# Optimization experiments

Hardware: AMD Instinct MI355X
Metric: run time of the kernel (lower is better)

The kernel has to match this reference:

```python
import jax, jax.numpy as jnp
import numpy as np

EMBED_DIM = 1024
NUM_HEADS = 16
HEAD_DIM = EMBED_DIM // NUM_HEADS
B, S = 2, 2048


def setup_inputs() -> dict:
    key = jax.random.key(0)
    ks = jax.random.split(key, 9)
    d = EMBED_DIM
    scale = 1.0 / np.sqrt(d)
    inp = {
        "x": jax.random.normal(ks[0], (B, S, d), dtype=jnp.float32),
        "mask": jnp.ones((B, S), dtype=jnp.int32),
        "Wq": jax.random.normal(ks[1], (d, d), dtype=jnp.float32) * scale,
        "bq": jnp.zeros((d,), dtype=jnp.float32),
        "Wk": jax.random.normal(ks[2], (d, d), dtype=jnp.float32) * scale,
        "bk": jnp.zeros((d,), dtype=jnp.float32),
        "Wv": jax.random.normal(ks[3], (d, d), dtype=jnp.float32) * scale,
        "bv": jnp.zeros((d,), dtype=jnp.float32),
        "Wo": jax.random.normal(ks[4], (d, d), dtype=jnp.float32) * scale,
        "bo": jnp.zeros((d,), dtype=jnp.float32),
    }
    return inp


def reference(x, mask, Wq, bq, Wk, bk, Wv, bv, Wo, bo):
    b, s, _ = x.shape
    # projections; torch Linear computes x @ W.T + b
    q = (x @ Wq.T + bq).reshape(b, s, NUM_HEADS, HEAD_DIM).transpose(0, 2, 1, 3)
    k = (x @ Wk.T + bk).reshape(b, s, NUM_HEADS, HEAD_DIM).transpose(0, 2, 1, 3)
    v = (x @ Wv.T + bv).reshape(b, s, NUM_HEADS, HEAD_DIM).transpose(0, 2, 1, 3)
    scores = jnp.einsum("bhqd,bhkd->bhqk", q, k) / np.sqrt(HEAD_DIM)  # (B,H,S,S)
    m = (mask == 0)[:, None, None, :]  # broadcast over heads and query pos
    scores = jnp.where(m, jnp.float32(-1e9), scores)
    attn = jax.nn.softmax(scores, axis=-1)
    out = jnp.einsum("bhqk,bhkd->bhqd", attn, v)
    out = out.transpose(0, 2, 1, 3).reshape(b, s, EMBED_DIM)
    return out @ Wo.T + bo
```

## Files before the change

### kernel.cpp

```cpp
#include <hip/hip_runtime.h>

#define EMBED 1024
#define NHEAD 16
#define HDIM  64
#define BB    2
#define SS    2048

typedef __bf16 bf16x8 __attribute__((ext_vector_type(8)));
typedef float  f32x4  __attribute__((ext_vector_type(4)));
typedef _Float16 f16x8 __attribute__((ext_vector_type(8)));
typedef __fp16 hf16x2 __attribute__((ext_vector_type(2)));

#if defined(__has_builtin)
#if __has_builtin(__builtin_amdgcn_exp2f)
#define EXP2(x) __builtin_amdgcn_exp2f(x)
#else
#define EXP2(x) exp2f(x)
#endif
#else
#define EXP2(x) exp2f(x)
#endif

__device__ __forceinline__ unsigned short f2bf(float f) {
  union { float f; unsigned u; } v; v.f = f;
  unsigned r = v.u + 0x7fffu + ((v.u >> 16) & 1u);
  return (unsigned short)(r >> 16);
}

__device__ __forceinline__ float bf2f(unsigned short u) {
  union { unsigned u; float f; } v; v.u = ((unsigned)u) << 16;
  return v.f;
}

__device__ __forceinline__ unsigned short f2h(float f) {
  union { _Float16 h; unsigned short u; } t;
  t.h = (_Float16)f;
  return t.u;
}

__device__ __forceinline__ void g2l16(const unsigned short* g, unsigned short* l) {
  __builtin_amdgcn_global_load_lds(
      (const __attribute__((address_space(1))) unsigned int*)g,
      (__attribute__((address_space(3))) unsigned int*)l, 16, 0, 0);
}

__global__ __launch_bounds__(256)
void cvt5_kernel(const float* __restrict__ x,  const float* __restrict__ Wq,
                 const float* __restrict__ Wk, const float* __restrict__ Wv,
                 const float* __restrict__ Wo, const int* __restrict__ mask,
                 unsigned short* __restrict__ xb,  unsigned short* __restrict__ Wqb,
                 unsigned short* __restrict__ Wkb, unsigned short* __restrict__ Wvb,
                 unsigned short* __restrict__ Wob, float* __restrict__ mbias) {
  const int i = blockIdx.x * 256 + threadIdx.x;
  if (i < (1 << 21)) {
    const float* src;
    unsigned short* dst;
    int j;
    if (i < (1 << 20)) {
      src = x; dst = xb; j = i;
    } else {
      const int t = i - (1 << 20);
      const int r = t >> 18;
      j = t & ((1 << 18) - 1);
      src = (r == 0) ? Wq : (r == 1) ? Wk : (r == 2) ? Wv : Wo;
      dst = (r == 0) ? Wqb : (r == 1) ? Wkb : (r == 2) ? Wvb : Wob;
    }
    const float4 f = ((const float4*)src)[j];
    ushort4 u;
    u.x = f2bf(f.x); u.y = f2bf(f.y); u.z = f2bf(f.z); u.w = f2bf(f.w);
    ((ushort4*)dst)[j] = u;
  } else {
    const int j = i - (1 << 21);
    const int4 m = ((const int4*)mask)[j];
    float4 o;
    o.x = m.x ? 0.f : -1e30f; o.y = m.y ? 0.f : -1e30f;
    o.z = m.z ? 0.f : -1e30f; o.w = m.w ? 0.f : -1e30f;
    ((float4*)mbias)[j] = o;
  }
}

template <typename EpiFn>
__device__ __forceinline__
void gemm_core(const unsigned short* __restrict__ A,
               const unsigned short* __restrict__ Bm,
               int m0, int n0, EpiFn epi) {
  __shared__ unsigned short sA[128 * 64];
  __shared__ unsigned short sB[128 * 64];
  const int tid = threadIdx.x;
  const int l  = tid & 63;
  const int w  = tid >> 6;
  const int lm = l & 15;
  const int qd = l >> 4;
  const int wm = w & 1;
  const int wn = w >> 1;

  f32x4 acc[4][4];
#pragma unroll
  for (int i = 0; i < 4; ++i)
#pragma unroll
    for (int j = 0; j < 4; ++j) acc[i][j] = (f32x4){0.f, 0.f, 0.f, 0.f};

  for (int k0 = 0; k0 < EMBED; k0 += 64) {
#pragma unroll
    for (int i = 0; i < 4; ++i) {
      const int t = i * 256 + tid;
      const int r = t >> 3;
      const int c = (t & 7) ^ (r & 7);
      g2l16(A + (m0 + r) * EMBED + k0 + c * 8, &sA[(i * 256 + (w << 6)) * 8]);
      g2l16(Bm + (n0 + r) * EMBED + k0 + c * 8, &sB[(i * 256 + (w << 6)) * 8]);
    }
    __syncthreads();
#pragma unroll
    for (int kk = 0; kk < 2; ++kk) {
      bf16x8 af[4], bfr[4];
#pragma unroll
      for (int mi = 0; mi < 4; ++mi) {
        const int R = wm * 64 + mi * 16 + lm;
        const int ch = R * 8 + (((kk << 2) + qd) ^ (R & 7));
        af[mi] = *(const bf16x8*)&sA[ch * 8];
      }
#pragma unroll
      for (int ni = 0; ni < 4; ++ni) {
        const int R = wn * 64 + ni * 16 + lm;
        const int ch = R * 8 + (((kk << 2) + qd) ^ (R & 7));
        bfr[ni] = *(const bf16x8*)&sB[ch * 8];
      }
#pragma unroll
      for (int mi = 0; mi < 4; ++mi)
#pragma unroll
        for (int ni = 0; ni < 4; ++ni)
          acc[mi][ni] = __builtin_amdgcn_mfma_f32_16x16x32_bf16(
              af[mi], bfr[ni], acc[mi][ni], 0, 0, 0);
    }
    __syncthreads();
  }

#pragma unroll
  for (int mi = 0; mi < 4; ++mi)
#pragma unroll
    for (int ni = 0; ni < 4; ++ni) {
      const int mb = m0 + wm * 64 + mi * 16 + qd * 4;
      const int n  = n0 + wn * 64 + ni * 16 + lm;
      epi(acc[mi][ni], mb, n);
    }
}

__device__ __forceinline__ void decode_tile(int flat, int& a0, int& b0) {
  const int sub = flat & 15;
  const int g = flat >> 4;
  a0 = ((g >> 2) * 2 + (sub >> 3));
  b0 = ((g & 3) * 8 + (sub & 7));
}

__global__ __launch_bounds__(256)
void gemm_qkv(const unsigned short* __restrict__ xb,
              const unsigned short* __restrict__ Wqb,
              const unsigned short* __restrict__ Wkb,
              const unsigned short* __restrict__ Wvb,
              const float* __restrict__ bq, const float* __restrict__ bk,
              const float* __restrict__ bv,
              unsigned short* __restrict__ Qb, unsigned short* __restrict__ Kb,
              unsigned short* __restrict__ VTb) {
  const int z = blockIdx.y;
  int a0, b0;
  decode_tile(blockIdx.x, a0, b0);
  if (z < 2) {
    const unsigned short* A = z ? Wkb : Wqb;
    const float* bias = z ? bk : bq;
    unsigned short* O = z ? Kb : Qb;
    const float scale = z ? 1.0f : 0.125f * 1.4426950408889634f;
    gemm_core(A, xb, a0 * 128, b0 * 128, [&](const f32x4& v, int mb, int n) {
      const float4 bvv = *(const float4*)&bias[mb];
      const int h = mb >> 6, d0 = mb & 63;
      const int b = n >> 11, s = n & 2047;
      int sw = s;
      if (z == 1)
        sw = (s & ~31) | (((s >> 2) & 1) << 4) | (((s >> 3) & 3) << 2) | (s & 3);
      ushort4 u;
      u.x = f2bf((v.x + bvv.x) * scale); u.y = f2bf((v.y + bvv.y) * scale);
      u.z = f2bf((v.z + bvv.z) * scale); u.w = f2bf((v.w + bvv.w) * scale);
      *(ushort4*)&O[(((b * NHEAD + h) * SS) + sw) * HDIM + d0] = u;
    });
  } else {
    gemm_core(xb, Wvb, b0 * 128, a0 * 128, [&](const f32x4& v, int mb, int n) {
      const float bvv = bv[n];
      const int b = mb >> 11, s = mb & 2047;
      const int h = n >> 6, d = n & 63;
      ushort4 u;
      u.x = f2h(v.x + bvv); u.y = f2h(v.y + bvv);
      u.z = f2h(v.z + bvv); u.w = f2h(v.w + bvv);
      *(ushort4*)&VTb[(((b * NHEAD + h) * HDIM) + d) * SS + s] = u;
    });
  }
}

__global__ __launch_bounds__(256)
void gemm_out(const unsigned short* __restrict__ Wob,
              const unsigned short* __restrict__ Ob,
              const float* __restrict__ bo, float* __restrict__ out) {
  int a0, b0;
  decode_tile(blockIdx.x, a0, b0);
  gemm_core(Wob, Ob, a0 * 128, b0 * 128, [&](const f32x4& v, int mb, int n) {
    const float4 bvv = *(const float4*)&bo[mb];
    float4 o;
    o.x = v.x + bvv.x; o.y = v.y + bvv.y; o.z = v.z + bvv.z; o.w = v.w + bvv.w;
    *(float4*)&out[n * EMBED + mb] = o;
  });
}

__global__ __launch_bounds__(256, 6)
void attn_kernel(const unsigned short* __restrict__ Q,
                 const unsigned short* __restrict__ K,
                 const unsigned short* __restrict__ VT,
                 const float* __restrict__ mbias,
                 unsigned short* __restrict__ Opart,
                 float* __restrict__ Lpart) {
  __shared__ unsigned short sK[64 * 64];
  __shared__ unsigned short sV[64 * 64];
  __shared__ float sMB[SS / 2];
  const int tid = threadIdx.x;
  const int l = tid & 63, w = tid >> 6;
  const int lm = l & 15, qd = l >> 4;
  const int b = blockIdx.z & 1, sp = blockIdx.z >> 1, h = blockIdx.y;
  const int q0 = blockIdx.x * 64 + w * 16;
  const unsigned short* Qh = Q + ((b * NHEAD + h) * SS) * HDIM;
  const unsigned short* Kh = K + ((b * NHEAD + h) * SS) * HDIM;
  const unsigned short* Vh = VT + ((b * NHEAD + h) * HDIM) * SS;
  const float* mb = mbias + b * SS + sp * (SS / 2);
  unsigned short* Op = Opart + sp * (BB * SS * EMBED);
  float* Lp = Lpart + sp * (BB * NHEAD * SS);
  const int kb0 = sp * (SS / 2);

  bf16x8 qf[2];
  qf[0] = *(const bf16x8*)&Qh[(q0 + lm) * HDIM + qd * 8];
  qf[1] = *(const bf16x8*)&Qh[(q0 + lm) * HDIM + 32 + qd * 8];

  auto stageKV = [&](int kb) {
#pragma unroll
    for (int i = 0; i < 2; ++i) {
      const int t = i * 256 + tid;
      const int r = t >> 3;
      const int c = (t & 7) ^ (r & 7);
      g2l16(Kh + (kb + r) * HDIM + c * 8, &sK[(i * 256 + (w << 6)) * 8]);
      g2l16(Vh + r * SS + kb + c * 8, &sV[(i * 256 + (w << 6)) * 8]);
    }
  };

  g2l16((const unsigned short*)(mb + tid * 4), (unsigned short*)&sMB[w * 256]);

  f32x4 Od[4];
#pragma unroll
  for (int i = 0; i < 4; ++i) Od[i] = (f32x4){0.f, 0.f, 0.f, 0.f};
  float lsum = 0.f;

  const int NT = (SS / 2) / 64;
  for (int t = 0; t < NT; ++t) {
    stageKV(kb0 + t * 64);
    __syncthreads();

#pragma unroll
    for (int p = 0; p < 2; ++p) {
      union PK { hf16x2 h2[4]; f16x8 v; } pk;
#pragma unroll
      for (int jj = 0; jj < 2; ++jj) {
        const int j = p * 2 + jj;
        const int R = j * 16 + lm;
        const bf16x8 k0 = *(const bf16x8*)&sK[(R * 8 + (qd ^ (lm & 7))) * 8];
        const bf16x8 k1 = *(const bf16x8*)&sK[(R * 8 + ((4 + qd) ^ (lm & 7))) * 8];
        const float4 bj = *(const float4*)&sMB[t * 64 + p * 32 + qd * 8 + jj * 4];
        f32x4 t0 = (f32x4){bj.x, bj.y, bj.z, bj.w};
        __builtin_amdgcn_s_setprio(1);
        t0 = __builtin_amdgcn_mfma_f32_16x16x32_bf16(k0, qf[0], t0, 0, 0, 0);
        t0 = __builtin_amdgcn_mfma_f32_16x16x32_bf16(k1, qf[1], t0, 0, 0, 0);
        __builtin_amdgcn_s_setprio(0);
        const float p0 = EXP2(t0[0]);
        const float p1 = EXP2(t0[1]);
        const float p2 = EXP2(t0[2]);
        const float p3 = EXP2(t0[3]);
        lsum += (p0 + p1) + (p2 + p3);
        pk.h2[jj * 2] = __builtin_amdgcn_cvt_pkrtz(p0, p1);
        pk.h2[jj * 2 + 1] = __builtin_amdgcn_cvt_pkrtz(p2, p3);
      }
      const f16x8 pf8 = pk.v;
      __builtin_amdgcn_s_setprio(1);
#pragma unroll
      for (int dt = 0; dt < 4; ++dt) {
        const f16x8 vf =
            *(const f16x8*)&sV[(dt * 16 + lm) * 64 + ((p * 4 + qd) ^ (lm & 7)) * 8];
        Od[dt] = __builtin_amdgcn_mfma_f32_16x16x32_f16(vf, pf8, Od[dt], 0, 0, 0);
      }
      __builtin_amdgcn_s_setprio(0);
    }
    __syncthreads();
  }

  float ls = lsum;
  ls += __shfl_xor(ls, 16);
  ls += __shfl_xor(ls, 32);
  if (qd == 0) Lp[(b * NHEAD + h) * SS + q0 + lm] = ls;
#pragma unroll
  for (int dt = 0; dt < 4; ++dt) {
    ushort4 u;
    u.x = f2bf(Od[dt][0]); u.y = f2bf(Od[dt][1]);
    u.z = f2bf(Od[dt][2]); u.w = f2bf(Od[dt][3]);
    *(ushort4*)&Op[(b * SS + q0 + lm) * EMBED + h * HDIM + dt * 16 + qd * 4] = u;
  }
}

__global__ __launch_bounds__(256)
void combine_kernel(const unsigned short* __restrict__ Opart,
                    const float* __restrict__ Lpart,
                    unsigned short* __restrict__ Ob) {
  const int i = blockIdx.x * 256 + threadIdx.x;
  const int base = i * 8;
  const int token = base >> 10;
  const int h = (base >> 6) & 15;
  const int b = token >> 11, q = token & 2047;
  const int lidx = (b * NHEAD + h) * SS + q;
  const float ls = Lpart[lidx] + Lpart[BB * NHEAD * SS + lidx];
  const float rinv = 1.f / ls;
  const ushort4* p0 = (const ushort4*)&Opart[base];
  const ushort4* p1 = (const ushort4*)&Opart[BB * SS * EMBED + base];
  ushort4 o[2];
#pragma unroll
  for (int k = 0; k < 2; ++k) {
    const ushort4 a = p0[k], c = p1[k];
    o[k].x = f2bf((bf2f(a.x) + bf2f(c.x)) * rinv);
    o[k].y = f2bf((bf2f(a.y) + bf2f(c.y)) * rinv);
    o[k].z = f2bf((bf2f(a.z) + bf2f(c.z)) * rinv);
    o[k].w = f2bf((bf2f(a.w) + bf2f(c.w)) * rinv);
  }
  *(ushort4*)&Ob[base] = o[0];
  *(ushort4*)&Ob[base + 4] = o[1];
}

extern "C" void kernel_launch(void* const* d_in, const int* in_sizes, int n_in,
                              void* d_out, int out_size, void* d_ws, size_t ws_size,
                              hipStream_t stream) {
  const float* x  = (const float*)d_in[0];
  const int* mask = (const int*)d_in[1];
  const float* Wq = (const float*)d_in[2];
  const float* bq = (const float*)d_in[3];
  const float* Wk = (const float*)d_in[4];
  const float* bk = (const float*)d_in[5];
  const float* Wv = (const float*)d_in[6];
  const float* bv = (const float*)d_in[7];
  const float* Wo = (const float*)d_in[8];
  const float* bo = (const float*)d_in[9];
  float* out = (float*)d_out;

  char* ws = (char*)d_ws;
  const size_t MB = 1024 * 1024;
  unsigned short* xb  = (unsigned short*)(ws);
  unsigned short* Ob  = (unsigned short*)(ws);
  unsigned short* Wqb = (unsigned short*)(ws + 8 * MB);
  unsigned short* Wkb = Wqb + 1024 * 1024;
  unsigned short* Wvb = Wkb + 1024 * 1024;
  unsigned short* Wob = Wvb + 1024 * 1024;
  unsigned short* Qb  = (unsigned short*)(ws + 16 * MB);
  unsigned short* Kb  = (unsigned short*)(ws + 24 * MB);
  unsigned short* VTb = (unsigned short*)(ws + 32 * MB);
  unsigned short* Opart = (unsigned short*)(ws + 40 * MB);
  float* mbb   = (float*)(ws + 56 * MB);
  float* Lpart = (float*)(ws + 56 * MB + 64 * 1024);

  cvt5_kernel<<<8196, 256, 0, stream>>>(x, Wq, Wk, Wv, Wo, mask,
                                        xb, Wqb, Wkb, Wvb, Wob, mbb);
  gemm_qkv<<<dim3(256, 3), 256, 0, stream>>>(xb, Wqb, Wkb, Wvb, bq, bk, bv,
                                             Qb, Kb, VTb);
  attn_kernel<<<dim3(32, 16, 4), 256, 0, stream>>>(Qb, Kb, VTb, mbb,
                                                   Opart, Lpart);
  combine_kernel<<<2048, 256, 0, stream>>>(Opart, Lpart, Ob);
  gemm_out<<<256, 256, 0, stream>>>(Wob, Ob, bo, out);
}
```

Before: 208.3 us.

## Fuse split-KV combine into output projection GEMM B-operand load

Removes the separate combine kernel. The output GEMM now reads both attention partials and the partial softmax sums directly, normalizes them and writes the bf16 result into shared memory as its B tile. This saves one launch plus a write and re-read of the combined tensor. In exchange, every M-tile block redoes the combine for its N rows, 8 times in total. The GEMM also loses the async g2l path for B and the gemm_core pipeline, so loads now stall behind the ALU conversion work.

```diff
diff --git a/kernel.cpp b/kernel.cpp
--- a/kernel.cpp
+++ b/kernel.cpp
@@ -10,6 +10,7 @@
 typedef float  f32x4  __attribute__((ext_vector_type(4)));
 typedef _Float16 f16x8 __attribute__((ext_vector_type(8)));
 typedef __fp16 hf16x2 __attribute__((ext_vector_type(2)));
+typedef unsigned short u16x8 __attribute__((ext_vector_type(8)));
 
 #if defined(__has_builtin)
 #if __has_builtin(__builtin_amdgcn_exp2f)
@@ -196,16 +197,93 @@
 
 __global__ __launch_bounds__(256)
 void gemm_out(const unsigned short* __restrict__ Wob,
-              const unsigned short* __restrict__ Ob,
+              const unsigned short* __restrict__ Opart,
+              const float* __restrict__ Lpart,
               const float* __restrict__ bo, float* __restrict__ out) {
+  __shared__ unsigned short sA[128 * 64];
+  __shared__ unsigned short sB[128 * 64];
   int a0, b0;
   decode_tile(blockIdx.x, a0, b0);
-  gemm_core(Wob, Ob, a0 * 128, b0 * 128, [&](const f32x4& v, int mb, int n) {
-    const float4 bvv = *(const float4*)&bo[mb];
-    float4 o;
-    o.x = v.x + bvv.x; o.y = v.y + bvv.y; o.z = v.z + bvv.z; o.w = v.w + bvv.w;
-    *(float4*)&out[n * EMBED + mb] = o;
-  });
+  const int m0 = a0 * 128, n0 = b0 * 128;
+  const int tid = threadIdx.x;
+  const int l  = tid & 63;
+  const int w  = tid >> 6;
+  const int lm = l & 15;
+  const int qd = l >> 4;
+  const int wm = w & 1;
+  const int wn = w >> 1;
+
+  f32x4 acc[4][4];
+#pragma unroll
+  for (int i = 0; i < 4; ++i)
+#pragma unroll
+    for (int j = 0; j < 4; ++j) acc[i][j] = (f32x4){0.f, 0.f, 0.f, 0.f};
+
+  for (int k0 = 0; k0 < EMBED; k0 += 64) {
+    const int h = k0 >> 6;
+#pragma unroll
+    for (int i = 0; i < 4; ++i) {
+      const int t = i * 256 + tid;
+      const int r = t >> 3;
+      const int c = (t & 7) ^ (r & 7);
+      g2l16(Wob + (m0 + r) * EMBED + k0 + c * 8, &sA[(i * 256 + (w << 6)) * 8]);
+    }
+#pragma unroll
+    for (int i = 0; i < 4; ++i) {
+      const int t = i * 256 + tid;
+      const int r = t >> 3;
+      const int c = (t & 7) ^ (r & 7);
+      const int n = n0 + r;
+      const int bb = n >> 11, q = n & 2047;
+      const int lidx = (bb * NHEAD + h) * SS + q;
+      const float rinv = 1.f / (Lpart[lidx] + Lpart[BB * NHEAD * SS + lidx]);
+      const u16x8 pa = *(const u16x8*)&Opart[n * EMBED + k0 + c * 8];
+      const u16x8 pb =
+          *(const u16x8*)&Opart[BB * SS * EMBED + n * EMBED + k0 + c * 8];
+      u16x8 o;
+#pragma unroll
+      for (int e = 0; e < 8; ++e)
+        o[e] = f2bf((bf2f(pa[e]) + bf2f(pb[e])) * rinv);
+      *(u16x8*)&sB[(i * 256 + tid) * 8] = o;
+    }
+    __syncthreads();
+#pragma unroll
+    for (int kk = 0; kk < 2; ++kk) {
+      bf16x8 af[4], bfr[4];
+#pragma unroll
+      for (int mi = 0; mi < 4; ++mi) {
+        const int R = wm * 64 + mi * 16 + lm;
+        const int ch = R * 8 + (((kk << 2) + qd) ^ (R & 7));
+        af[mi] = *(const bf16x8*)&sA[ch * 8];
+      }
+#pragma unroll
+      for (int ni = 0; ni < 4; ++ni) {
+        const int R = wn * 64 + ni * 16 + lm;
+        const int ch = R * 8 + (((kk << 2) + qd) ^ (R & 7));
+        bfr[ni] = *(const bf16x8*)&sB[ch * 8];
+      }
+#pragma unroll
+      for (int mi = 0; mi < 4; ++mi)
+#pragma unroll
+        for (int ni = 0; ni < 4; ++ni)
+          acc[mi][ni] = __builtin_amdgcn_mfma_f32_16x16x32_bf16(
+              af[mi], bfr[ni], acc[mi][ni], 0, 0, 0);
+    }
+    __syncthreads();
+  }
+
+#pragma unroll
+  for (int mi = 0; mi < 4; ++mi)
+#pragma unroll
+    for (int ni = 0; ni < 4; ++ni) {
+      const int mb = m0 + wm * 64 + mi * 16 + qd * 4;
+      const int n  = n0 + wn * 64 + ni * 16 + lm;
+      const float4 bvv = *(const float4*)&bo[mb];
+      float4 o;
+      o.x = acc[mi][ni][0] + bvv.x; o.y = acc[mi][ni][1] + bvv.y;
+      o.z = acc[mi][ni][2] + bvv.z; o.w = acc[mi][ni][3] + bvv.w;
+      *(float4*)&out[n * EMBED + mb] = o;
+    }
 }
 
 __global__ __launch_bounds__(256, 6)
@@ -307,33 +385,6 @@
   }
 }
 
-__global__ __launch_bounds__(256)
-void combine_kernel(const unsigned short* __restrict__ Opart,
-                    const float* __restrict__ Lpart,
-                    unsigned short* __restrict__ Ob) {
-  const int i = blockIdx.x * 256 + threadIdx.x;
-  const int base = i * 8;
-  const int token = base >> 10;
-  const int h = (base >> 6) & 15;
-  const int b = token >> 11, q = token & 2047;
-  const int lidx = (b * NHEAD + h) * SS + q;
-  const float ls = Lpart[lidx] + Lpart[BB * NHEAD * SS + lidx];
-  const float rinv = 1.f / ls;
-  const ushort4* p0 = (const ushort4*)&Opart[base];
-  const ushort4* p1 = (const ushort4*)&Opart[BB * SS * EMBED + base];
-  ushort4 o[2];
-#pragma unroll
-  for (int k = 0; k < 2; ++k) {
-    const ushort4 a = p0[k], c = p1[k];
-    o[k].x = f2bf((bf2f(a.x) + bf2f(c.x)) * rinv);
-    o[k].y = f2bf((bf2f(a.y) + bf2f(c.y)) * rinv);
-    o[k].z = f2bf((bf2f(a.z) + bf2f(c.z)) * rinv);
-    o[k].w = f2bf((bf2f(a.w) + bf2f(c.w)) * rinv);
-  }
-  *(ushort4*)&Ob[base] = o[0];
-  *(ushort4*)&Ob[base + 4] = o[1];
-}
-
 extern "C" void kernel_launch(void* const* d_in, const int* in_sizes, int n_in,
                               void* d_out, int out_size, void* d_ws, size_t ws_size,
                               hipStream_t stream) {
@@ -352,7 +403,6 @@
   char* ws = (char*)d_ws;
   const size_t MB = 1024 * 1024;
   unsigned short* xb  = (unsigned short*)(ws);
-  unsigned short* Ob  = (unsigned short*)(ws);
   unsigned short* Wqb = (unsigned short*)(ws + 8 * MB);
   unsigned short* Wkb = Wqb + 1024 * 1024;
   unsigned short* Wvb = Wkb + 1024 * 1024;
@@ -370,6 +420,5 @@
                                              Qb, Kb, VTb);
   attn_kernel<<<dim3(32, 16, 4), 256, 0, stream>>>(Qb, Kb, VTb, mbb,
                                                    Opart, Lpart);
-  combine_kernel<<<2048, 256, 0, stream>>>(Opart, Lpart, Ob);
-  gemm_out<<<256, 256, 0, stream>>>(Wob, Ob, bo, out);
-}
+  gemm_out<<<256, 256, 0, stream>>>(Wob, Opart, Lpart, bo, out);
+}
```

Result: slower. 227.0 us (+9.0%).

## Halve GEMM M-tile to 64 and remap block IDs for XCD-aware scheduling

Applied to the files above, without the earlier changes.

GEMM tiles shrink from 128x128 to 64x128, doubling the block count of the QKV and output projections (256 to 512 per GEMM) so the 256-CU MI355X gets a fuller wave. Block indices in the GEMMs and the attention kernel are remapped with a (bid&7)*N + bid>>3 permutation, so blocks landing on the same XCD share neighbouring tiles and get better L2 reuse. The cost is lower per-block arithmetic intensity, since each B tile is loaded twice as often, and smaller MFMA accumulator tiles per wave.

```diff
diff --git a/kernel.cpp b/kernel.cpp
--- a/kernel.cpp
+++ b/kernel.cpp
@@ -81,10 +81,10 @@
 
 template <typename EpiFn>
 __device__ __forceinline__
-void gemm_core(const unsigned short* __restrict__ A,
-               const unsigned short* __restrict__ Bm,
-               int m0, int n0, EpiFn epi) {
-  __shared__ unsigned short sA[128 * 64];
+void gemm_core64(const unsigned short* __restrict__ A,
+                 const unsigned short* __restrict__ Bm,
+                 int m0, int n0, EpiFn epi) {
+  __shared__ unsigned short sA[64 * 64];
   __shared__ unsigned short sB[128 * 64];
   const int tid = threadIdx.x;
   const int l  = tid & 63;
@@ -94,28 +94,34 @@
   const int wm = w & 1;
   const int wn = w >> 1;
 
-  f32x4 acc[4][4];
-#pragma unroll
-  for (int i = 0; i < 4; ++i)
+  f32x4 acc[2][4];
+#pragma unroll
+  for (int i = 0; i < 2; ++i)
 #pragma unroll
     for (int j = 0; j < 4; ++j) acc[i][j] = (f32x4){0.f, 0.f, 0.f, 0.f};
 
   for (int k0 = 0; k0 < EMBED; k0 += 64) {
+#pragma unroll
+    for (int i = 0; i < 2; ++i) {
+      const int t = i * 256 + tid;
+      const int r = t >> 3;
+      const int c = (t & 7) ^ (r & 7);
+      g2l16(A + (m0 + r) * EMBED + k0 + c * 8, &sA[(i * 256 + (w << 6)) * 8]);
+    }
 #pragma unroll
     for (int i = 0; i < 4; ++i) {
       const int t = i * 256 + tid;
       const int r = t >> 3;
       const int c = (t & 7) ^ (r & 7);
-      g2l16(A + (m0 + r) * EMBED + k0 + c * 8, &sA[(i * 256 + (w << 6)) * 8]);
       g2l16(Bm + (n0 + r) * EMBED + k0 + c * 8, &sB[(i * 256 + (w << 6)) * 8]);
     }
     __syncthreads();
 #pragma unroll
     for (int kk = 0; kk < 2; ++kk) {
-      bf16x8 af[4], bfr[4];
-#pragma unroll
-      for (int mi = 0; mi < 4; ++mi) {
-        const int R = wm * 64 + mi * 16 + lm;
+      bf16x8 af[2], bfr[4];
+#pragma unroll
+      for (int mi = 0; mi < 2; ++mi) {
+        const int R = wm * 32 + mi * 16 + lm;
         const int ch = R * 8 + (((kk << 2) + qd) ^ (R & 7));
         af[mi] = *(const bf16x8*)&sA[ch * 8];
       }
@@ -126,7 +132,7 @@
         bfr[ni] = *(const bf16x8*)&sB[ch * 8];
       }
 #pragma unroll
-      for (int mi = 0; mi < 4; ++mi)
+      for (int mi = 0; mi < 2; ++mi)
 #pragma unroll
         for (int ni = 0; ni < 4; ++ni)
           acc[mi][ni] = __builtin_amdgcn_mfma_f32_16x16x32_bf16(
@@ -136,20 +142,13 @@
   }
 
 #pragma unroll
-  for (int mi = 0; mi < 4; ++mi)
+  for (int mi = 0; mi < 2; ++mi)
 #pragma unroll
     for (int ni = 0; ni < 4; ++ni) {
-      const int mb = m0 + wm * 64 + mi * 16 + qd * 4;
+      const int mb = m0 + wm * 32 + mi * 16 + qd * 4;
       const int n  = n0 + wn * 64 + ni * 16 + lm;
       epi(acc[mi][ni], mb, n);
     }
-}
-
-__device__ __forceinline__ void decode_tile(int flat, int& a0, int& b0) {
-  const int sub = flat & 15;
-  const int g = flat >> 4;
-  a0 = ((g >> 2) * 2 + (sub >> 3));
-  b0 = ((g & 3) * 8 + (sub & 7));
 }
 
 __global__ __launch_bounds__(256)
@@ -162,14 +161,16 @@
               unsigned short* __restrict__ Qb, unsigned short* __restrict__ Kb,
               unsigned short* __restrict__ VTb) {
   const int z = blockIdx.y;
-  int a0, b0;
-  decode_tile(blockIdx.x, a0, b0);
+  const int bid = blockIdx.x;
+  const int lg = (bid & 7) * 64 + (bid >> 3);
   if (z < 2) {
     const unsigned short* A = z ? Wkb : Wqb;
     const float* bias = z ? bk : bq;
     unsigned short* O = z ? Kb : Qb;
     const float scale = z ? 1.0f : 0.125f * 1.4426950408889634f;
-    gemm_core(A, xb, a0 * 128, b0 * 128, [&](const f32x4& v, int mb, int n) {
+    const int m0 = (lg & 15) * 64;
+    const int n0 = (lg >> 4) * 128;
+    gemm_core64(A, xb, m0, n0, [&](const f32x4& v, int mb, int n) {
       const float4 bvv = *(const float4*)&bias[mb];
       const int h = mb >> 6, d0 = mb & 63;
       const int b = n >> 11, s = n & 2047;
@@ -182,7 +183,9 @@
       *(ushort4*)&O[(((b * NHEAD + h) * SS) + sw) * HDIM + d0] = u;
     });
   } else {
-    gemm_core(xb, Wvb, b0 * 128, a0 * 128, [&](const f32x4& v, int mb, int n) {
+    const int m0 = (lg & 63) * 64;
+    const int n0 = (lg >> 6) * 128;
+    gemm_core64(xb, Wvb, m0, n0, [&](const f32x4& v, int mb, int n) {
       const float bvv = bv[n];
       const int b = mb >> 11, s = mb & 2047;
       const int h = n >> 6, d = n & 63;
@@ -198,9 +201,11 @@
 void gemm_out(const unsigned short* __restrict__ Wob,
               const unsigned short* __restrict__ Ob,
               const float* __restrict__ bo, float* __restrict__ out) {
-  int a0, b0;
-  decode_tile(blockIdx.x, a0, b0);
-  gemm_core(Wob, Ob, a0 * 128, b0 * 128, [&](const f32x4& v, int mb, int n) {
+  const int bid = blockIdx.x;
+  const int lg = (bid & 7) * 64 + (bid >> 3);
+  const int m0 = (lg & 15) * 64;
+  const int n0 = (lg >> 4) * 128;
+  gemm_core64(Wob, Ob, m0, n0, [&](const f32x4& v, int mb, int n) {
     const float4 bvv = *(const float4*)&bo[mb];
     float4 o;
     o.x = v.x + bvv.x; o.y = v.y + bvv.y; o.z = v.z + bvv.z; o.w = v.w + bvv.w;
@@ -221,8 +226,13 @@
   const int tid = threadIdx.x;
   const int l = tid & 63, w = tid >> 6;
   const int lm = l & 15, qd = l >> 4;
-  const int b = blockIdx.z & 1, sp = blockIdx.z >> 1, h = blockIdx.y;
-  const int q0 = blockIdx.x * 64 + w * 16;
+  const int bid = blockIdx.x;
+  const int lg = (bid & 7) * 256 + (bid >> 3);
+  const int qt = lg & 31;
+  const int h  = (lg >> 5) & 15;
+  const int zz = lg >> 9;
+  const int b = zz & 1, sp = zz >> 1;
+  const int q0 = qt * 64 + w * 16;
   const unsigned short* Qh = Q + ((b * NHEAD + h) * SS) * HDIM;
   const unsigned short* Kh = K + ((b * NHEAD + h) * SS) * HDIM;
   const unsigned short* Vh = VT + ((b * NHEAD + h) * HDIM) * SS;
@@ -366,10 +376,9 @@
 
   cvt5_kernel<<<8196, 256, 0, stream>>>(x, Wq, Wk, Wv, Wo, mask,
                                         xb, Wqb, Wkb, Wvb, Wob, mbb);
-  gemm_qkv<<<dim3(256, 3), 256, 0, stream>>>(xb, Wqb, Wkb, Wvb, bq, bk, bv,
+  gemm_qkv<<<dim3(512, 3), 256, 0, stream>>>(xb, Wqb, Wkb, Wvb, bq, bk, bv,
                                              Qb, Kb, VTb);
-  attn_kernel<<<dim3(32, 16, 4), 256, 0, stream>>>(Qb, Kb, VTb, mbb,
-                                                   Opart, Lpart);
+  attn_kernel<<<2048, 256, 0, stream>>>(Qb, Kb, VTb, mbb, Opart, Lpart);
   combine_kernel<<<2048, 256, 0, stream>>>(Opart, Lpart, Ob);
-  gemm_out<<<256, 256, 0, stream>>>(Wob, Ob, bo, out);
-}
+  gemm_out<<<512, 256, 0, stream>>>(Wob, Ob, bo, out);
+}
```

After: 198.8 us. 4.6% less time.
